# Performance work log

Measured on AMD Instinct MI355X. Metric: run time of the kernel, lower is better.

## Reference

```python
import jax, jax.numpy as jnp
import numpy as np

N_NODES = 25000
N_EDGES = 400000
IN_DIM, HID_DIM, OUT_DIM = 174, 128, 64


def setup_inputs() -> dict:
    key = jax.random.key(0)
    ks = jax.random.split(key, 8)
    x = jax.random.normal(ks[0], (N_NODES, IN_DIM), dtype=jnp.float32)
    edge_index = jax.random.randint(ks[1], (2, N_EDGES), 0, N_NODES, dtype=jnp.int64)
    # PyG SAGEConv params: lin_l (neighbors, with bias), lin_r (root, no bias)
    def glorot(k, shape):
        lim = float(np.sqrt(6.0 / (shape[0] + shape[1])))
        return jax.random.uniform(k, shape, jnp.float32, -lim, lim)
    W1_l = glorot(ks[2], (HID_DIM, IN_DIM))
    W1_r = glorot(ks[3], (HID_DIM, IN_DIM))
    b1 = jnp.zeros((HID_DIM,), jnp.float32)
    W2_l = glorot(ks[4], (OUT_DIM, HID_DIM))
    W2_r = glorot(ks[5], (OUT_DIM, HID_DIM))
    b2 = jnp.zeros((OUT_DIM,), jnp.float32)
    return {"x": x, "edge_index": edge_index, "W1_l": W1_l, "b1": b1,
            "W1_r": W1_r, "W2_l": W2_l, "b2": b2, "W2_r": W2_r}


def _sage_conv(h, src, dst, W_l, b, W_r):
    # mean-aggregate neighbor features at destination nodes
    msg = h[src]                                       # [E, F] gather
    summed = jax.ops.segment_sum(msg, dst, num_segments=N_NODES)  # [N, F]
    deg = jax.ops.segment_sum(jnp.ones((src.shape[0],), h.dtype), dst,
                              num_segments=N_NODES)    # [N]
    mean = summed / jnp.maximum(deg, 1.0)[:, None]
    # out = lin_l(mean) + lin_r(h)
    return mean @ W_l.T + b + h @ W_r.T


def reference(x, edge_index, W1_l, b1, W1_r, W2_l, b2, W2_r):
    src, dst = edge_index[0], edge_index[1]
    h = _sage_conv(x, src, dst, W1_l, b1, W1_r)
    h = jax.nn.relu(h)
    # dropout is identity in eval mode (module exposes freeze() for inference)
    out = _sage_conv(h, src, dst, W2_l, b2, W2_r)
    return out
```

## Files before the change

### kernel.cpp

```cpp
#include <hip/hip_runtime.h>

#define N_NODES 25000
#define N_EDGES 400000
#define IN_DIM 174
#define HID_DIM 128
#define OUT_DIM 64
#define MPAD 25088
#define BINCAP 64

using u32 = unsigned int;
typedef __attribute__((ext_vector_type(8))) short s16x8;
typedef __attribute__((ext_vector_type(4))) float f32x4;

__device__ __forceinline__ float bflo(u32 u) { u32 t = u << 16; return __builtin_bit_cast(float, t); }
__device__ __forceinline__ float bfhi(u32 u) { u32 t = u & 0xffff0000u; return __builtin_bit_cast(float, t); }
__device__ __forceinline__ u32 f2b(float f) {
    u32 u = __builtin_bit_cast(u32, f);
    return (u + 0x7fffu + ((u >> 16) & 1u)) >> 16;
}
__device__ __forceinline__ u32 packbf2(float a, float b) { return f2b(a) | (f2b(b) << 16); }

__device__ __forceinline__ void gload_lds16(const void* g, void* l) {
    __builtin_amdgcn_global_load_lds(
        (const __attribute__((address_space(1))) u32*)g,
        (__attribute__((address_space(3))) u32*)l, 16, 0, 0);
}

#define XB_CNT (N_NODES * 96)
#define WB1_CNT (256 * 96)
#define WB2_CNT (128 * 64)
#define PREP_TOT (XB_CNT + WB1_CNT + WB2_CNT + N_NODES)

__global__ __launch_bounds__(256) void prep_all_kernel(
    const float* __restrict__ x,
    const float* __restrict__ W1l, const float* __restrict__ W1r,
    const float* __restrict__ W2l, const float* __restrict__ W2r,
    u32* __restrict__ xb, u32* __restrict__ wb1, u32* __restrict__ wb2,
    int* __restrict__ degI) {
    int idx = blockIdx.x * blockDim.x + threadIdx.x;
    if (idx < XB_CNT) {
        int n = idx / 96, d2 = idx - n * 96;
        float2 v = make_float2(0.f, 0.f);
        if (d2 < 87) v = ((const float2*)(x + (size_t)n * IN_DIM))[d2];
        xb[idx] = packbf2(v.x, v.y);
        return;
    }
    idx -= XB_CNT;
    if (idx < WB1_CNT) {
        int nrow = idx / 96, d2 = idx - nrow * 96;
        const float* src = (nrow < 128) ? W1l + (size_t)nrow * IN_DIM
                                        : W1r + (size_t)(nrow - 128) * IN_DIM;
        float2 v = make_float2(0.f, 0.f);
        if (d2 < 87) v = ((const float2*)src)[d2];
        wb1[idx] = packbf2(v.x, v.y);
        return;
    }
    idx -= WB1_CNT;
    if (idx < WB2_CNT) {
        int nrow = idx >> 6, d2 = idx & 63;
        const float* src = (nrow < 64) ? W2l + (size_t)nrow * HID_DIM
                                       : W2r + (size_t)(nrow - 64) * HID_DIM;
        float2 v = ((const float2*)src)[d2];
        wb2[idx] = packbf2(v.x, v.y);
        return;
    }
    idx -= WB2_CNT;
    if (idx < N_NODES) degI[idx] = 0;
}

__global__ void fill_bin_kernel(const int* __restrict__ ei, int* __restrict__ degI,
                                int* __restrict__ bins) {
    int e = blockIdx.x * blockDim.x + threadIdx.x;
    if (e < N_EDGES) {
        int src = ei[e];
        int dst = ei[N_EDGES + e];
        int pos = atomicAdd(&degI[dst], 1);
        if (pos < BINCAP) bins[dst * BINCAP + pos] = src;
    }
}

template <int K, int NSPLIT>
__global__ __launch_bounds__(256) void gemm_mfma(const ushort* __restrict__ A,
                                                 const ushort* __restrict__ B,
                                                 ushort* __restrict__ Cn,
                                                 ushort* __restrict__ Cr) {
    __shared__ ushort As[128 * 32];
    __shared__ ushort Bs[128 * 32];
    const int tid = threadIdx.x;
    const int lane = tid & 63, w = tid >> 6;
    const int m0 = blockIdx.x * 128;
    const int n0 = blockIdx.y * 128;
    const int wm = w >> 1, wn = w & 1;

    f32x4 acc[4][4] = {};

    const int arow = lane >> 2;
    const int achunk = (lane & 3) * 8;

    for (int kk = 0; kk < K; kk += 32) {
        #pragma unroll
        for (int c = 0; c < 2; ++c) {
            int r = w * 32 + c * 16;
            gload_lds16(A + (size_t)(m0 + r + arow) * K + kk + achunk, &As[r * 32]);
            gload_lds16(B + (size_t)(n0 + r + arow) * K + kk + achunk, &Bs[r * 32]);
        }
        __syncthreads();
        s16x8 af[4], bf[4];
        const int fr = lane & 15, fo = (lane >> 4) * 8;
        #pragma unroll
        for (int i = 0; i < 4; ++i) {
            af[i] = *(const s16x8*)&As[(wm * 64 + i * 16 + fr) * 32 + fo];
            bf[i] = *(const s16x8*)&Bs[(wn * 64 + i * 16 + fr) * 32 + fo];
        }
        #pragma unroll
        for (int i = 0; i < 4; ++i)
            #pragma unroll
            for (int j = 0; j < 4; ++j)
                acc[i][j] = __builtin_amdgcn_mfma_f32_16x16x32_bf16(af[i], bf[j], acc[i][j], 0, 0, 0);
        __syncthreads();
    }

    const int cr = (lane >> 4) * 4, cc = lane & 15;
    #pragma unroll
    for (int i = 0; i < 4; ++i)
        #pragma unroll
        for (int r = 0; r < 4; ++r) {
            int row = m0 + wm * 64 + i * 16 + cr + r;
            #pragma unroll
            for (int j = 0; j < 4; ++j) {
                int colg = n0 + wn * 64 + j * 16 + cc;
                ushort* Cp = (colg < NSPLIT) ? Cn : Cr;
                int c = (colg < NSPLIT) ? colg : colg - NSPLIT;
                Cp[(size_t)row * NSPLIT + c] = (ushort)f2b(acc[i][j][r]);
            }
        }
}

__global__ __launch_bounds__(256) void agg1_kernel(const u32* __restrict__ y1n,
                                                   const u32* __restrict__ y1r,
                                                   const int* __restrict__ degI,
                                                   const int* __restrict__ bins,
                                                   const float* __restrict__ b1,
                                                   u32* __restrict__ h1) {
    int w = threadIdx.x >> 6, lane = threadIdx.x & 63;
    int n = blockIdx.x * 4 + w;
    if (n >= N_NODES) return;
    int deg = degI[n];
    int d = min(deg, BINCAP);
    const int* bp = bins + n * BINCAP;
    float a0 = 0.f, a1 = 0.f;
    int j = 0;
    for (; j + 4 <= d; j += 4) {
        int4 s4 = *(const int4*)(bp + j);
        u32 u0 = y1n[(size_t)s4.x * 64 + lane];
        u32 u1 = y1n[(size_t)s4.y * 64 + lane];
        u32 u2 = y1n[(size_t)s4.z * 64 + lane];
        u32 u3 = y1n[(size_t)s4.w * 64 + lane];
        a0 += bflo(u0) + bflo(u1) + bflo(u2) + bflo(u3);
        a1 += bfhi(u0) + bfhi(u1) + bfhi(u2) + bfhi(u3);
    }
    for (; j < d; ++j) {
        int s = bp[j];
        u32 u = y1n[(size_t)s * 64 + lane];
        a0 += bflo(u); a1 += bfhi(u);
    }
    float inv = 1.f / fmaxf((float)deg, 1.f);
    u32 ur = y1r[(size_t)n * 64 + lane];
    float2 bb = ((const float2*)b1)[lane];
    float v0 = fmaxf(a0 * inv + bflo(ur) + bb.x, 0.f);
    float v1 = fmaxf(a1 * inv + bfhi(ur) + bb.y, 0.f);
    h1[(size_t)n * 64 + lane] = packbf2(v0, v1);
}

__global__ __launch_bounds__(256) void agg2_kernel(const u32* __restrict__ y2n,
                                                   const u32* __restrict__ y2r,
                                                   const int* __restrict__ degI,
                                                   const int* __restrict__ bins,
                                                   const float* __restrict__ b2,
                                                   float2* __restrict__ out) {
    int w = threadIdx.x >> 6, lane = threadIdx.x & 63;
    int half = lane >> 5, dd = lane & 31;
    int n = blockIdx.x * 4 + w;
    if (n >= N_NODES) return;
    int deg = degI[n];
    int d = min(deg, BINCAP);
    const int* bp = bins + n * BINCAP;
    float a0 = 0.f, a1 = 0.f;
    int j = 0;
    for (; j + 4 <= d; j += 4) {
        int s0 = bp[j + half], s1 = bp[j + 2 + half];
        u32 u0 = y2n[(size_t)s0 * 32 + dd];
        u32 u1 = y2n[(size_t)s1 * 32 + dd];
        a0 += bflo(u0) + bflo(u1);
        a1 += bfhi(u0) + bfhi(u1);
    }
    if (j + 2 <= d) {
        int s = bp[j + half];
        u32 u = y2n[(size_t)s * 32 + dd];
        a0 += bflo(u); a1 += bfhi(u);
        j += 2;
    }
    if (j < d && half == 0) {
        int s = bp[j];
        u32 u = y2n[(size_t)s * 32 + dd];
        a0 += bflo(u); a1 += bfhi(u);
    }
    a0 += __shfl_xor(a0, 32, 64);
    a1 += __shfl_xor(a1, 32, 64);
    if (half == 0) {
        float inv = 1.f / fmaxf((float)deg, 1.f);
        u32 ur = y2r[(size_t)n * 32 + dd];
        float2 bb = ((const float2*)b2)[dd];
        float2 o;
        o.x = a0 * inv + bflo(ur) + bb.x;
        o.y = a1 * inv + bfhi(ur) + bb.y;
        out[(size_t)n * 32 + dd] = o;
    }
}


extern "C" void kernel_launch(void* const* d_in, const int* in_sizes, int n_in,
                              void* d_out, int out_size, void* d_ws, size_t ws_size,
                              hipStream_t stream) {
    const float* x   = (const float*)d_in[0];
    const int*   ei  = (const int*)d_in[1];
    const float* W1l = (const float*)d_in[2];
    const float* b1  = (const float*)d_in[3];
    const float* W1r = (const float*)d_in[4];
    const float* W2l = (const float*)d_in[5];
    const float* b2  = (const float*)d_in[6];
    const float* W2r = (const float*)d_in[7];

    char* w = (char*)d_ws;
    auto alloc = [&](size_t bytes) -> char* {
        char* p = w;
        w += (bytes + 255) & ~(size_t)255;
        return p;
    };
    int* degI = (int*)alloc((size_t)N_NODES * 4);
    int* bins = (int*)alloc((size_t)N_NODES * BINCAP * 4);
    u32* wb1  = (u32*)alloc((size_t)WB1_CNT * 4);
    u32* wb2  = (u32*)alloc((size_t)WB2_CNT * 4);
    u32* xb   = (u32*)alloc((size_t)MPAD * 96 * 4);
    u32* y1n  = (u32*)alloc((size_t)MPAD * 64 * 4);
    u32* y1r  = (u32*)alloc((size_t)MPAD * 64 * 4);
    u32* y2n  = (u32*)alloc((size_t)MPAD * 32 * 4);
    u32* y2r  = (u32*)alloc((size_t)MPAD * 32 * 4);
    u32* h1   = xb;

    prep_all_kernel<<<(PREP_TOT + 255) / 256, 256, 0, stream>>>(
        x, W1l, W1r, W2l, W2r, xb, wb1, wb2, degI);
    fill_bin_kernel<<<(N_EDGES + 255) / 256, 256, 0, stream>>>(ei, degI, bins);

    gemm_mfma<192, 128><<<dim3(196, 2), 256, 0, stream>>>(
        (const ushort*)xb, (const ushort*)wb1, (ushort*)y1n, (ushort*)y1r);
    agg1_kernel<<<(N_NODES + 3) / 4, 256, 0, stream>>>(y1n, y1r, degI, bins, b1, h1);
    gemm_mfma<128, 64><<<dim3(196, 1), 256, 0, stream>>>(
        (const ushort*)h1, (const ushort*)wb2, (ushort*)y2n, (ushort*)y2r);
    agg2_kernel<<<(N_NODES + 3) / 4, 256, 0, stream>>>(y2n, y2r, degI, bins, b2, (float2*)d_out);
}
```

Before: 89.66 us.

## Vectorize prep/edge binning, shrink GEMM2 M-tile, deepen aggregation unrolling

The x-to-bf16 conversion now handles four packed pairs per thread and writes them as 128-bit stores. Edge binning processes two edges per thread using int2 loads. The second GEMM is templated to a 64-row M tile so twice as many blocks run on the small second-layer problem. Both aggregation kernels unroll the neighbor gather to eight edges per iteration for more memory-level parallelism, which costs extra registers.

```diff
diff --git a/kernel.cpp b/kernel.cpp
--- a/kernel.cpp
+++ b/kernel.cpp
@@ -11,6 +11,7 @@
 using u32 = unsigned int;
 typedef __attribute__((ext_vector_type(8))) short s16x8;
 typedef __attribute__((ext_vector_type(4))) float f32x4;
+typedef __attribute__((ext_vector_type(4))) u32 u32x4;
 
 __device__ __forceinline__ float bflo(u32 u) { u32 t = u << 16; return __builtin_bit_cast(float, t); }
 __device__ __forceinline__ float bfhi(u32 u) { u32 t = u & 0xffff0000u; return __builtin_bit_cast(float, t); }
@@ -26,10 +27,10 @@
         (__attribute__((address_space(3))) u32*)l, 16, 0, 0);
 }
 
-#define XB_CNT (N_NODES * 96)
+#define XB4_CNT (N_NODES * 24)
 #define WB1_CNT (256 * 96)
 #define WB2_CNT (128 * 64)
-#define PREP_TOT (XB_CNT + WB1_CNT + WB2_CNT + N_NODES)
+#define PREP_TOT (XB4_CNT + WB1_CNT + WB2_CNT + N_NODES)
 
 __global__ __launch_bounds__(256) void prep_all_kernel(
     const float* __restrict__ x,
@@ -38,14 +39,21 @@
     u32* __restrict__ xb, u32* __restrict__ wb1, u32* __restrict__ wb2,
     int* __restrict__ degI) {
     int idx = blockIdx.x * blockDim.x + threadIdx.x;
-    if (idx < XB_CNT) {
-        int n = idx / 96, d2 = idx - n * 96;
-        float2 v = make_float2(0.f, 0.f);
-        if (d2 < 87) v = ((const float2*)(x + (size_t)n * IN_DIM))[d2];
-        xb[idx] = packbf2(v.x, v.y);
+    if (idx < XB4_CNT) {
+        int n = idx / 24, d8 = idx - n * 24;
+        const float* xr = x + (size_t)n * IN_DIM;
+        u32x4 o;
+        #pragma unroll
+        for (int q = 0; q < 4; ++q) {
+            int d2 = d8 * 4 + q;
+            float2 v = make_float2(0.f, 0.f);
+            if (d2 < 87) v = ((const float2*)xr)[d2];
+            o[q] = packbf2(v.x, v.y);
+        }
+        *(u32x4*)(xb + (size_t)n * 96 + d8 * 4) = o;
         return;
     }
-    idx -= XB_CNT;
+    idx -= XB4_CNT;
     if (idx < WB1_CNT) {
         int nrow = idx / 96, d2 = idx - nrow * 96;
         const float* src = (nrow < 128) ? W1l + (size_t)nrow * IN_DIM
@@ -70,50 +78,59 @@
 
 __global__ void fill_bin_kernel(const int* __restrict__ ei, int* __restrict__ degI,
                                 int* __restrict__ bins) {
-    int e = blockIdx.x * blockDim.x + threadIdx.x;
-    if (e < N_EDGES) {
-        int src = ei[e];
-        int dst = ei[N_EDGES + e];
-        int pos = atomicAdd(&degI[dst], 1);
-        if (pos < BINCAP) bins[dst * BINCAP + pos] = src;
-    }
-}
-
-template <int K, int NSPLIT>
+    int e2 = (blockIdx.x * blockDim.x + threadIdx.x) * 2;
+    if (e2 < N_EDGES) {
+        int2 s = *(const int2*)(ei + e2);
+        int2 t = *(const int2*)(ei + N_EDGES + e2);
+        int p0 = atomicAdd(&degI[t.x], 1);
+        if (p0 < BINCAP) bins[t.x * BINCAP + p0] = s.x;
+        int p1 = atomicAdd(&degI[t.y], 1);
+        if (p1 < BINCAP) bins[t.y * BINCAP + p1] = s.y;
+    }
+}
+
+template <int K, int NSPLIT, int BM>
 __global__ __launch_bounds__(256) void gemm_mfma(const ushort* __restrict__ A,
                                                  const ushort* __restrict__ B,
                                                  ushort* __restrict__ Cn,
                                                  ushort* __restrict__ Cr) {
-    __shared__ ushort As[128 * 32];
+    constexpr int MI = BM / 32;
+    __shared__ ushort As[BM * 32];
     __shared__ ushort Bs[128 * 32];
     const int tid = threadIdx.x;
     const int lane = tid & 63, w = tid >> 6;
-    const int m0 = blockIdx.x * 128;
+    const int m0 = blockIdx.x * BM;
     const int n0 = blockIdx.y * 128;
-    const int wm = w >> 1, wn = w & 1;
-
-    f32x4 acc[4][4] = {};
+    const int wmo = (w >> 1) * (MI * 16);
+    const int wno = (w & 1) * 64;
+
+    f32x4 acc[MI][4] = {};
 
     const int arow = lane >> 2;
     const int achunk = (lane & 3) * 8;
 
     for (int kk = 0; kk < K; kk += 32) {
         #pragma unroll
+        for (int c = 0; c < BM / 64; ++c) {
+            int r = w * (BM / 4) + c * 16;
+            gload_lds16(A + (size_t)(m0 + r + arow) * K + kk + achunk, &As[r * 32]);
+        }
+        #pragma unroll
         for (int c = 0; c < 2; ++c) {
             int r = w * 32 + c * 16;
-            gload_lds16(A + (size_t)(m0 + r + arow) * K + kk + achunk, &As[r * 32]);
             gload_lds16(B + (size_t)(n0 + r + arow) * K + kk + achunk, &Bs[r * 32]);
         }
         __syncthreads();
-        s16x8 af[4], bf[4];
+        s16x8 af[MI], bf[4];
         const int fr = lane & 15, fo = (lane >> 4) * 8;
         #pragma unroll
-        for (int i = 0; i < 4; ++i) {
-            af[i] = *(const s16x8*)&As[(wm * 64 + i * 16 + fr) * 32 + fo];
-            bf[i] = *(const s16x8*)&Bs[(wn * 64 + i * 16 + fr) * 32 + fo];
-        }
-        #pragma unroll
-        for (int i = 0; i < 4; ++i)
+        for (int i = 0; i < MI; ++i)
+            af[i] = *(const s16x8*)&As[(wmo + i * 16 + fr) * 32 + fo];
+        #pragma unroll
+        for (int j = 0; j < 4; ++j)
+            bf[j] = *(const s16x8*)&Bs[(wno + j * 16 + fr) * 32 + fo];
+        #pragma unroll
+        for (int i = 0; i < MI; ++i)
             #pragma unroll
             for (int j = 0; j < 4; ++j)
                 acc[i][j] = __builtin_amdgcn_mfma_f32_16x16x32_bf16(af[i], bf[j], acc[i][j], 0, 0, 0);
@@ -122,13 +139,13 @@
 
     const int cr = (lane >> 4) * 4, cc = lane & 15;
     #pragma unroll
-    for (int i = 0; i < 4; ++i)
+    for (int i = 0; i < MI; ++i)
         #pragma unroll
         for (int r = 0; r < 4; ++r) {
-            int row = m0 + wm * 64 + i * 16 + cr + r;
+            int row = m0 + wmo + i * 16 + cr + r;
             #pragma unroll
             for (int j = 0; j < 4; ++j) {
-                int colg = n0 + wn * 64 + j * 16 + cc;
+                int colg = n0 + wno + j * 16 + cc;
                 ushort* Cp = (colg < NSPLIT) ? Cn : Cr;
                 int c = (colg < NSPLIT) ? colg : colg - NSPLIT;
                 Cp[(size_t)row * NSPLIT + c] = (ushort)f2b(acc[i][j][r]);
@@ -150,7 +167,23 @@
     const int* bp = bins + n * BINCAP;
     float a0 = 0.f, a1 = 0.f;
     int j = 0;
-    for (; j + 4 <= d; j += 4) {
+    for (; j + 8 <= d; j += 8) {
+        int4 sa = *(const int4*)(bp + j);
+        int4 sb = *(const int4*)(bp + j + 4);
+        u32 u0 = y1n[(size_t)sa.x * 64 + lane];
+        u32 u1 = y1n[(size_t)sa.y * 64 + lane];
+        u32 u2 = y1n[(size_t)sa.z * 64 + lane];
+        u32 u3 = y1n[(size_t)sa.w * 64 + lane];
+        u32 u4 = y1n[(size_t)sb.x * 64 + lane];
+        u32 u5 = y1n[(size_t)sb.y * 64 + lane];
+        u32 u6 = y1n[(size_t)sb.z * 64 + lane];
+        u32 u7 = y1n[(size_t)sb.w * 64 + lane];
+        a0 += bflo(u0) + bflo(u1) + bflo(u2) + bflo(u3)
+            + bflo(u4) + bflo(u5) + bflo(u6) + bflo(u7);
+        a1 += bfhi(u0) + bfhi(u1) + bfhi(u2) + bfhi(u3)
+            + bfhi(u4) + bfhi(u5) + bfhi(u6) + bfhi(u7);
+    }
+    if (j + 4 <= d) {
         int4 s4 = *(const int4*)(bp + j);
         u32 u0 = y1n[(size_t)s4.x * 64 + lane];
         u32 u1 = y1n[(size_t)s4.y * 64 + lane];
@@ -158,6 +191,7 @@
         u32 u3 = y1n[(size_t)s4.w * 64 + lane];
         a0 += bflo(u0) + bflo(u1) + bflo(u2) + bflo(u3);
         a1 += bfhi(u0) + bfhi(u1) + bfhi(u2) + bfhi(u3);
+        j += 4;
     }
     for (; j < d; ++j) {
         int s = bp[j];
@@ -187,12 +221,23 @@
     const int* bp = bins + n * BINCAP;
     float a0 = 0.f, a1 = 0.f;
     int j = 0;
-    for (; j + 4 <= d; j += 4) {
+    for (; j + 8 <= d; j += 8) {
+        int s0 = bp[j + half],     s1 = bp[j + 2 + half];
+        int s2 = bp[j + 4 + half], s3 = bp[j + 6 + half];
+        u32 u0 = y2n[(size_t)s0 * 32 + dd];
+        u32 u1 = y2n[(size_t)s1 * 32 + dd];
+        u32 u2 = y2n[(size_t)s2 * 32 + dd];
+        u32 u3 = y2n[(size_t)s3 * 32 + dd];
+        a0 += bflo(u0) + bflo(u1) + bflo(u2) + bflo(u3);
+        a1 += bfhi(u0) + bfhi(u1) + bfhi(u2) + bfhi(u3);
+    }
+    if (j + 4 <= d) {
         int s0 = bp[j + half], s1 = bp[j + 2 + half];
         u32 u0 = y2n[(size_t)s0 * 32 + dd];
         u32 u1 = y2n[(size_t)s1 * 32 + dd];
         a0 += bflo(u0) + bflo(u1);
         a1 += bfhi(u0) + bfhi(u1);
+        j += 4;
     }
     if (j + 2 <= d) {
         int s = bp[j + half];
@@ -250,12 +295,12 @@
 
     prep_all_kernel<<<(PREP_TOT + 255) / 256, 256, 0, stream>>>(
         x, W1l, W1r, W2l, W2r, xb, wb1, wb2, degI);
-    fill_bin_kernel<<<(N_EDGES + 255) / 256, 256, 0, stream>>>(ei, degI, bins);
-
-    gemm_mfma<192, 128><<<dim3(196, 2), 256, 0, stream>>>(
+    fill_bin_kernel<<<(N_EDGES / 2 + 255) / 256, 256, 0, stream>>>(ei, degI, bins);
+
+    gemm_mfma<192, 128, 128><<<dim3(196, 2), 256, 0, stream>>>(
         (const ushort*)xb, (const ushort*)wb1, (ushort*)y1n, (ushort*)y1r);
     agg1_kernel<<<(N_NODES + 3) / 4, 256, 0, stream>>>(y1n, y1r, degI, bins, b1, h1);
-    gemm_mfma<128, 64><<<dim3(196, 1), 256, 0, stream>>>(
+    gemm_mfma<128, 64, 64><<<dim3(392, 1), 256, 0, stream>>>(
         (const ushort*)h1, (const ushort*)wb2, (ushort*)y2n, (ushort*)y2r);
     agg2_kernel<<<(N_NODES + 3) / 4, 256, 0, stream>>>(y2n, y2r, degI, bins, b2, (float2*)d_out);
 }
```

New measurement: 83.39 us. -7.0%, faster.
